# Kernel optimization log

Hardware: AMD Instinct MI355X
Metric: run time of the kernel (lower is better)

The kernel has to match this reference:

```python
import jax, jax.numpy as jnp
import numpy as np

ALPHA = 0.25
GAMMA = 2.0
EPS = 1e-8


def _pairwise_giou_loss(pred, true):
    # pred: (b,1,N,4), true: (b,m,1,4); boxes in [y1,x1,y2,x2] (tfa convention)
    py1, px1, py2, px2 = [pred[..., i] for i in range(4)]
    ty1, tx1, ty2, tx2 = [true[..., i] for i in range(4)]
    p_area = jnp.maximum(py2 - py1, 0.0) * jnp.maximum(px2 - px1, 0.0)
    t_area = jnp.maximum(ty2 - ty1, 0.0) * jnp.maximum(tx2 - tx1, 0.0)
    i_h = jnp.maximum(jnp.minimum(py2, ty2) - jnp.maximum(py1, ty1), 0.0)
    i_w = jnp.maximum(jnp.minimum(px2, tx2) - jnp.maximum(px1, tx1), 0.0)
    inter = i_h * i_w
    union = p_area + t_area - inter
    iou = jnp.where(union > 0, inter / jnp.maximum(union, EPS), 0.0)
    e_h = jnp.maximum(py2, ty2) - jnp.minimum(py1, ty1)
    e_w = jnp.maximum(px2, tx2) - jnp.minimum(px1, tx1)
    enclose = e_h * e_w
    giou = iou - jnp.where(enclose > 0, (enclose - union) / jnp.maximum(enclose, EPS), 0.0)
    return 1.0 - giou  # (b,m,N)


def setup_inputs():
    key = jax.random.key(0)
    k1, k2, k3, k4 = jax.random.split(key, 4)
    b, w, h, c, m = 8, 128, 128, 80, 100
    # probabilities in (0,1) as produced by a sigmoid head
    cls_pred = jax.random.uniform(k1, (b, w, h, c), jnp.float32, 1e-4, 1.0 - 1e-4)
    # raw box coords in grid units (divided by [w,h,w,h] inside the module)
    loc_pred = jax.random.uniform(k2, (b, w, h, 4), jnp.float32) * jnp.asarray([w, h, w, h], jnp.float32)
    labels = jax.random.randint(k3, (b, m), 0, c)
    cls_true = jax.nn.one_hot(labels, c, dtype=jnp.float32)
    loc_true = jax.random.uniform(k4, (b, m, 4), jnp.float32)
    reg_mask = jnp.ones((b, m), jnp.float32)
    return {"cls_pred": cls_pred, "loc_pred": loc_pred, "cls_true": cls_true,
            "loc_true": loc_true, "reg_mask": reg_mask}


def reference(cls_pred, loc_pred, cls_true, loc_true, reg_mask):
    b, w, h, c = cls_pred.shape
    m = cls_true.shape[1]
    cls_true = (cls_true == 1).astype(jnp.float32)
    p = cls_pred.reshape(b, w * h, c)                                      # (b,N,c)
    loc_p = loc_pred.reshape(b, w * h, 4) / jnp.asarray([w, h, w, h], jnp.float32)
    # focal-style pos/neg class costs; contract over c instead of materializing (b,m,N,c)
    neg = (1.0 - ALPHA) * p ** GAMMA * (-jnp.log(1.0 - p + EPS))
    pos = ALPHA * (1.0 - p) ** GAMMA * (-jnp.log(p + EPS))
    cls_loss = jnp.einsum('bnc,bmc->bmn', pos - neg, cls_true)             # (b,m,N)
    reg_loss = jnp.sum(jnp.abs(loc_true[:, :, None, :] - loc_p[:, None, :, :]), axis=-1)
    giou_loss = _pairwise_giou_loss(loc_p[:, None, :, :], loc_true[:, :, None, :])
    total = 2.0 * cls_loss + 5.0 * reg_loss + 2.0 * giou_loss              # (b,m,N)
    argmin_total = jnp.argmin(total, axis=-1).astype(jnp.int32)            # (b,m)
    batch_idx = jnp.broadcast_to(jnp.arange(b, dtype=jnp.int32)[:, None], (b, m))
    cls_id = jnp.argmax(cls_true, axis=-1).astype(jnp.int32)
    return jnp.stack([batch_idx, argmin_total, cls_id], axis=-1)           # (b,m,3) int32
```

## Files before the change

### kernel.cpp

```cpp
#include <hip/hip_runtime.h>
#include <stdint.h>

#define B    8
#define C    80
#define M    100
#define NPIX 16384
#define NT   32
#define BT   128
#define NW   4

#define ALPHA_F 0.25f
#define EPS_F   1e-8f

#define SWZ(c) ((((c) & 31)) ^ ((((c) >> 5)) << 3))

__device__ __forceinline__ uint32_t fkey(float f) {
    uint32_t u = __float_as_uint(f);
    return (u & 0x80000000u) ? ~u : (u | 0x80000000u);
}

__global__ __launch_bounds__(256) void init_kernel(
    const float* __restrict__ cls_true,
    int* __restrict__ cids,
    unsigned long long* __restrict__ keys)
{
    const int bm   = blockIdx.x * NW + (threadIdx.x >> 6);
    const int lane = threadIdx.x & 63;
    if (bm >= B * M) return;

    const float* ct = cls_true + (size_t)bm * C;
    const float v0 = ct[lane];
    unsigned long long k =
        ((unsigned long long)fkey(v0) << 32) | (unsigned int)(C - 1 - lane);
    if (lane + 64 < C) {
        const float v1 = ct[lane + 64];
        unsigned long long k1 =
            ((unsigned long long)fkey(v1) << 32) | (unsigned int)(C - 1 - (lane + 64));
        if (k1 > k) k = k1;
    }
    #pragma unroll
    for (int off = 32; off > 0; off >>= 1) {
        unsigned long long o = __shfl_xor(k, off, 64);
        if (o > k) k = o;
    }
    if (lane == 0) {
        cids[bm] = C - 1 - (int)(k & 0xFFFFFFFFull);
        keys[bm] = 0xFFFFFFFFFFFFFFFFull;
    }
}

__global__ __launch_bounds__(BT, 6) void match_kernel(
    const float* __restrict__ cls_pred,
    const float* __restrict__ loc_pred,
    const float* __restrict__ loc_true,
    const int*   __restrict__ cids,
    unsigned long long* __restrict__ keys)
{
#pragma clang fp contract(off)
    __shared__ float  D[C * NT];
    __shared__ float4 bx4[NT];
    __shared__ float  bpa[NT];

    const int b    = blockIdx.y;
    const int n0   = blockIdx.x * NT;
    const int tid  = threadIdx.x;
    const int lane = tid & 63;
    const int w    = tid >> 6;

    const float4* src4 = (const float4*)(cls_pred + ((size_t)b * NPIX + n0) * C);
    #pragma unroll
    for (int it = 0; it < NT * C / 4 / BT; ++it) {
        const int idx4 = it * BT + tid;
        const int n    = idx4 / 20;
        const int c0   = (idx4 - n * 20) * 4;
        const float4 v = src4[idx4];
        const float pv[4] = { v.x, v.y, v.z, v.w };
        #pragma unroll
        for (int jj = 0; jj < 4; ++jj) {
            const int c = c0 + jj;
            const float p = pv[jj];
            const float q = 1.0f - p;
            const float pos = (ALPHA_F * (q * q)) * (-logf(p + EPS_F));
            const float neg = ((1.0f - ALPHA_F) * (p * p)) * (-logf(q + EPS_F));
            D[c * NT + ((n ^ SWZ(c)) & (NT - 1))] = pos - neg;
        }
    }

    if (tid < NT) {
        const float inv = 1.0f / 128.0f;
        const float4 lp = *(const float4*)(loc_pred + ((size_t)b * NPIX + n0 + tid) * 4);
        const float py1 = lp.x * inv;
        const float px1 = lp.y * inv;
        const float py2 = lp.z * inv;
        const float px2 = lp.w * inv;
        bx4[tid] = make_float4(py1, px1, py2, px2);
        bpa[tid] = fmaxf(py2 - py1, 0.0f) * fmaxf(px2 - px1, 0.0f);
    }

    __syncthreads();

    const int mm = w * 64 + lane;
    if (mm < M) {
        const int bm  = b * M + mm;
        const int cid = cids[bm];
        const float4 lt = *(const float4*)(loc_true + (size_t)bm * 4);
        const float ty1 = lt.x, tx1 = lt.y, ty2 = lt.z, tx2 = lt.w;
        const float t_area = fmaxf(ty2 - ty1, 0.0f) * fmaxf(tx2 - tx1, 0.0f);

        const int drow = cid * NT;
        const int sw   = SWZ(cid) & (NT - 1);

        float bestv = __builtin_huge_valf();
        int   bestn = 0;

        #pragma unroll 8
        for (int j = 0; j < NT; ++j) {
            const float  d  = D[drow + (j ^ sw)];
            const float4 bx = bx4[j];
            const float  pa = bpa[j];
            const float py1 = bx.x, px1 = bx.y, py2 = bx.z, px2 = bx.w;

            const float r = ((fabsf(ty1 - py1) + fabsf(tx1 - px1))
                             + fabsf(ty2 - py2)) + fabsf(tx2 - px2);

            const float ih = fmaxf(fminf(py2, ty2) - fmaxf(py1, ty1), 0.0f);
            const float iw = fmaxf(fminf(px2, tx2) - fmaxf(px1, tx1), 0.0f);
            const float inter = ih * iw;
            const float uni   = (pa + t_area) - inter;
            const float iou   = (uni > 0.0f) ? (inter / fmaxf(uni, EPS_F)) : 0.0f;
            const float eh = fmaxf(py2, ty2) - fminf(py1, ty1);
            const float ew = fmaxf(px2, tx2) - fminf(px1, tx1);
            const float enc = eh * ew;
            const float pen = (enc > 0.0f) ? ((enc - uni) / fmaxf(enc, EPS_F)) : 0.0f;
            const float gl  = 1.0f - (iou - pen);

            const float total = ((2.0f * d) + (5.0f * r)) + (2.0f * gl);

            if (total < bestv) { bestv = total; bestn = n0 + j; }
        }

        const unsigned long long key =
            ((unsigned long long)fkey(bestv) << 32) | (unsigned int)bestn;
        atomicMin(&keys[bm], key);
    }
}

__global__ void write_out_kernel(const unsigned long long* __restrict__ keys,
                                 const int* __restrict__ cids,
                                 int* __restrict__ out) {
    int i = blockIdx.x * blockDim.x + threadIdx.x;
    if (i >= B * M) return;
    out[i * 3 + 0] = i / M;
    out[i * 3 + 1] = (int)(keys[i] & 0xFFFFFFFFull);
    out[i * 3 + 2] = cids[i];
}

extern "C" void kernel_launch(void* const* d_in, const int* in_sizes, int n_in,
                              void* d_out, int out_size, void* d_ws, size_t ws_size,
                              hipStream_t stream) {
    const float* cls_pred = (const float*)d_in[0];
    const float* loc_pred = (const float*)d_in[1];
    const float* cls_true = (const float*)d_in[2];
    const float* loc_true = (const float*)d_in[3];
    int* out = (int*)d_out;

    unsigned long long* keys = (unsigned long long*)d_ws;
    int* cids = (int*)((char*)d_ws + (size_t)B * M * sizeof(unsigned long long));

    init_kernel<<<(B * M + NW - 1) / NW, 256, 0, stream>>>(cls_true, cids, keys);
    match_kernel<<<dim3(NPIX / NT, B), BT, 0, stream>>>(
        cls_pred, loc_pred, loc_true, cids, keys);
    write_out_kernel<<<(B * M + 255) / 256, 256, 0, stream>>>(keys, cids, out);
}
```

Before: 65.78 us.

## Double-buffer class-cost tiles and precompute scaled pred boxes in prep kernel

Each block now handles two 32-pixel tiles. It loads the next tile's class probabilities into registers while it scores the current tile from a double-buffered shared array, so global load latency overlaps with the GIoU compute. Box scaling and area are moved into a separate prep kernel that writes padded 8-float records. The match loop reads those records directly from global memory instead of from shared memory. This adds a kernel launch and a workspace buffer, halves the grid size and drops the occupancy hint from the launch bounds.

```diff
diff --git a/kernel.cpp b/kernel.cpp
--- a/kernel.cpp
+++ b/kernel.cpp
@@ -6,6 +6,7 @@
 #define M    100
 #define NPIX 16384
 #define NT   32
+#define KT   2
 #define BT   128
 #define NW   4
 
@@ -49,96 +50,146 @@
     }
 }
 
-__global__ __launch_bounds__(BT, 6) void match_kernel(
+__global__ __launch_bounds__(256) void prep_kernel(
+    const float* __restrict__ loc_pred,
+    float* __restrict__ pbox)
+{
+#pragma clang fp contract(off)
+    const int i = blockIdx.x * 256 + threadIdx.x;
+    if (i >= B * NPIX) return;
+    const float inv = 1.0f / 128.0f;
+    const float4 lp = ((const float4*)loc_pred)[i];
+    const float py1 = lp.x * inv;
+    const float px1 = lp.y * inv;
+    const float py2 = lp.z * inv;
+    const float px2 = lp.w * inv;
+    const float pa  = fmaxf(py2 - py1, 0.0f) * fmaxf(px2 - px1, 0.0f);
+    float4* dst = (float4*)pbox + (size_t)i * 2;
+    dst[0] = make_float4(py1, px1, py2, px2);
+    dst[1] = make_float4(pa, 0.0f, 0.0f, 0.0f);
+}
+
+__global__ __launch_bounds__(BT) void match_kernel(
     const float* __restrict__ cls_pred,
-    const float* __restrict__ loc_pred,
+    const float* __restrict__ pbox,
     const float* __restrict__ loc_true,
     const int*   __restrict__ cids,
     unsigned long long* __restrict__ keys)
 {
 #pragma clang fp contract(off)
-    __shared__ float  D[C * NT];
-    __shared__ float4 bx4[NT];
-    __shared__ float  bpa[NT];
-
-    const int b    = blockIdx.y;
-    const int n0   = blockIdx.x * NT;
-    const int tid  = threadIdx.x;
-    const int lane = tid & 63;
-    const int w    = tid >> 6;
-
-    const float4* src4 = (const float4*)(cls_pred + ((size_t)b * NPIX + n0) * C);
+    __shared__ float D[2][C * NT];
+
+    const int b      = blockIdx.y;
+    const int base_n = blockIdx.x * (NT * KT);
+    const int tid    = threadIdx.x;
+    const int lane   = tid & 63;
+    const int w      = tid >> 6;
+
+    const int  mm  = w * 64 + lane;
+    const bool act = (mm < M);
+    const int  bm  = b * M + (act ? mm : 0);
+    int cid = 0, drow = 0, sw = 0;
+    float ty1 = 0.f, tx1 = 0.f, ty2 = 0.f, tx2 = 0.f, t_area = 0.f;
+    if (act) {
+        cid = cids[bm];
+        const float4 lt = *(const float4*)(loc_true + (size_t)bm * 4);
+        ty1 = lt.x; tx1 = lt.y; ty2 = lt.z; tx2 = lt.w;
+        t_area = fmaxf(ty2 - ty1, 0.0f) * fmaxf(tx2 - tx1, 0.0f);
+        drow = cid * NT;
+        sw   = SWZ(cid) & (NT - 1);
+    }
+
+    {
+        const float4* src4 = (const float4*)(cls_pred + ((size_t)b * NPIX + base_n) * C);
+        #pragma unroll
+        for (int it = 0; it < NT * C / 4 / BT; ++it) {
+            const int idx4 = it * BT + tid;
+            const int n    = idx4 / 20;
+            const int c0   = (idx4 - n * 20) * 4;
+            const float4 v = src4[idx4];
+            const float pv[4] = { v.x, v.y, v.z, v.w };
+            #pragma unroll
+            for (int jj = 0; jj < 4; ++jj) {
+                const int c = c0 + jj;
+                const float p = pv[jj];
+                const float q = 1.0f - p;
+                const float pos = (ALPHA_F * (q * q)) * (-logf(p + EPS_F));
+                const float neg = ((1.0f - ALPHA_F) * (p * p)) * (-logf(q + EPS_F));
+                D[0][c * NT + ((n ^ SWZ(c)) & (NT - 1))] = pos - neg;
+            }
+        }
+    }
+    __syncthreads();
+
+    float bestv = __builtin_huge_valf();
+    int   bestn = 0;
+
     #pragma unroll
-    for (int it = 0; it < NT * C / 4 / BT; ++it) {
-        const int idx4 = it * BT + tid;
-        const int n    = idx4 / 20;
-        const int c0   = (idx4 - n * 20) * 4;
-        const float4 v = src4[idx4];
-        const float pv[4] = { v.x, v.y, v.z, v.w };
-        #pragma unroll
-        for (int jj = 0; jj < 4; ++jj) {
-            const int c = c0 + jj;
-            const float p = pv[jj];
-            const float q = 1.0f - p;
-            const float pos = (ALPHA_F * (q * q)) * (-logf(p + EPS_F));
-            const float neg = ((1.0f - ALPHA_F) * (p * p)) * (-logf(q + EPS_F));
-            D[c * NT + ((n ^ SWZ(c)) & (NT - 1))] = pos - neg;
-        }
-    }
-
-    if (tid < NT) {
-        const float inv = 1.0f / 128.0f;
-        const float4 lp = *(const float4*)(loc_pred + ((size_t)b * NPIX + n0 + tid) * 4);
-        const float py1 = lp.x * inv;
-        const float px1 = lp.y * inv;
-        const float py2 = lp.z * inv;
-        const float px2 = lp.w * inv;
-        bx4[tid] = make_float4(py1, px1, py2, px2);
-        bpa[tid] = fmaxf(py2 - py1, 0.0f) * fmaxf(px2 - px1, 0.0f);
-    }
-
-    __syncthreads();
-
-    const int mm = w * 64 + lane;
-    if (mm < M) {
-        const int bm  = b * M + mm;
-        const int cid = cids[bm];
-        const float4 lt = *(const float4*)(loc_true + (size_t)bm * 4);
-        const float ty1 = lt.x, tx1 = lt.y, ty2 = lt.z, tx2 = lt.w;
-        const float t_area = fmaxf(ty2 - ty1, 0.0f) * fmaxf(tx2 - tx1, 0.0f);
-
-        const int drow = cid * NT;
-        const int sw   = SWZ(cid) & (NT - 1);
-
-        float bestv = __builtin_huge_valf();
-        int   bestn = 0;
-
-        #pragma unroll 8
-        for (int j = 0; j < NT; ++j) {
-            const float  d  = D[drow + (j ^ sw)];
-            const float4 bx = bx4[j];
-            const float  pa = bpa[j];
-            const float py1 = bx.x, px1 = bx.y, py2 = bx.z, px2 = bx.w;
-
-            const float r = ((fabsf(ty1 - py1) + fabsf(tx1 - px1))
-                             + fabsf(ty2 - py2)) + fabsf(tx2 - px2);
-
-            const float ih = fmaxf(fminf(py2, ty2) - fmaxf(py1, ty1), 0.0f);
-            const float iw = fmaxf(fminf(px2, tx2) - fmaxf(px1, tx1), 0.0f);
-            const float inter = ih * iw;
-            const float uni   = (pa + t_area) - inter;
-            const float iou   = (uni > 0.0f) ? (inter / fmaxf(uni, EPS_F)) : 0.0f;
-            const float eh = fmaxf(py2, ty2) - fminf(py1, ty1);
-            const float ew = fmaxf(px2, tx2) - fminf(px1, tx1);
-            const float enc = eh * ew;
-            const float pen = (enc > 0.0f) ? ((enc - uni) / fmaxf(enc, EPS_F)) : 0.0f;
-            const float gl  = 1.0f - (iou - pen);
-
-            const float total = ((2.0f * d) + (5.0f * r)) + (2.0f * gl);
-
-            if (total < bestv) { bestv = total; bestn = n0 + j; }
-        }
-
+    for (int t = 0; t < KT; ++t) {
+        const int cur = t & 1;
+        const int tn0 = base_n + t * NT;
+
+        float4 ld[5];
+        if (t + 1 < KT) {
+            const float4* src4 =
+                (const float4*)(cls_pred + ((size_t)b * NPIX + tn0 + NT) * C);
+            #pragma unroll
+            for (int it = 0; it < 5; ++it) ld[it] = src4[it * BT + tid];
+        }
+
+        if (act) {
+            const float* pb = pbox + ((size_t)(b * NPIX) + tn0) * 8;
+            #pragma unroll 8
+            for (int j = 0; j < NT; ++j) {
+                const float d   = D[cur][drow + (j ^ sw)];
+                const float py1 = pb[j * 8 + 0];
+                const float px1 = pb[j * 8 + 1];
+                const float py2 = pb[j * 8 + 2];
+                const float px2 = pb[j * 8 + 3];
+                const float pa  = pb[j * 8 + 4];
+
+                const float r = ((fabsf(ty1 - py1) + fabsf(tx1 - px1))
+                                 + fabsf(ty2 - py2)) + fabsf(tx2 - px2);
+
+                const float ih = fmaxf(fminf(py2, ty2) - fmaxf(py1, ty1), 0.0f);
+                const float iw = fmaxf(fminf(px2, tx2) - fmaxf(px1, tx1), 0.0f);
+                const float inter = ih * iw;
+                const float uni   = (pa + t_area) - inter;
+                const float iou   = (uni > 0.0f) ? (inter / fmaxf(uni, EPS_F)) : 0.0f;
+                const float eh = fmaxf(py2, ty2) - fminf(py1, ty1);
+                const float ew = fmaxf(px2, tx2) - fminf(px1, tx1);
+                const float enc = eh * ew;
+                const float pen = (enc > 0.0f) ? ((enc - uni) / fmaxf(enc, EPS_F)) : 0.0f;
+                const float gl  = 1.0f - (iou - pen);
+
+                const float total = ((2.0f * d) + (5.0f * r)) + (2.0f * gl);
+
+                if (total < bestv) { bestv = total; bestn = tn0 + j; }
+            }
+        }
+
+        if (t + 1 < KT) {
+            #pragma unroll
+            for (int it = 0; it < 5; ++it) {
+                const int idx4 = it * BT + tid;
+                const int n    = idx4 / 20;
+                const int c0   = (idx4 - n * 20) * 4;
+                const float pv[4] = { ld[it].x, ld[it].y, ld[it].z, ld[it].w };
+                #pragma unroll
+                for (int jj = 0; jj < 4; ++jj) {
+                    const int c = c0 + jj;
+                    const float p = pv[jj];
+                    const float q = 1.0f - p;
+                    const float pos = (ALPHA_F * (q * q)) * (-logf(p + EPS_F));
+                    const float neg = ((1.0f - ALPHA_F) * (p * p)) * (-logf(q + EPS_F));
+                    D[1 - cur][c * NT + ((n ^ SWZ(c)) & (NT - 1))] = pos - neg;
+                }
+            }
+            __syncthreads();
+        }
+    }
+
+    if (act) {
         const unsigned long long key =
             ((unsigned long long)fkey(bestv) << 32) | (unsigned int)bestn;
         atomicMin(&keys[bm], key);
@@ -165,10 +216,12 @@
     int* out = (int*)d_out;
 
     unsigned long long* keys = (unsigned long long*)d_ws;
-    int* cids = (int*)((char*)d_ws + (size_t)B * M * sizeof(unsigned long long));
+    int*   cids = (int*)((char*)d_ws + (size_t)B * M * sizeof(unsigned long long));
+    float* pbox = (float*)((char*)d_ws + 16384);
 
     init_kernel<<<(B * M + NW - 1) / NW, 256, 0, stream>>>(cls_true, cids, keys);
-    match_kernel<<<dim3(NPIX / NT, B), BT, 0, stream>>>(
-        cls_pred, loc_pred, loc_true, cids, keys);
+    prep_kernel<<<(B * NPIX + 255) / 256, 256, 0, stream>>>(loc_pred, pbox);
+    match_kernel<<<dim3(NPIX / (NT * KT), B), BT, 0, stream>>>(
+        cls_pred, pbox, loc_true, cids, keys);
     write_out_kernel<<<(B * M + 255) / 256, 256, 0, stream>>>(keys, cids, out);
 }
```

Result: faster. 60.33 us (-8.3%).

## Halve pixel tile, use row-major D, and load predicted boxes directly per thread

Applied to the files above, without the earlier changes.

The match kernel tile drops from 32 to 16 pixels per block, which doubles the grid. The swizzled column-major shared class-cost table is replaced by a plain [NT][C] row-major layout filled with float2 stores. The shared staging of predicted boxes and areas is removed, so each thread loads the loc_pred float4s itself (uniform across the wave) and recomputes the pixel area. The ground-truth setup is hoisted above the barrier and the inner loop is fully unrolled. In exchange there are twice as many atomicMin operations, redundant box loads across waves, and possible LDS bank conflicts on the per-thread gather D[j][cid].

```diff
diff --git a/kernel.cpp b/kernel.cpp
--- a/kernel.cpp
+++ b/kernel.cpp
@@ -5,14 +5,12 @@
 #define C    80
 #define M    100
 #define NPIX 16384
-#define NT   32
+#define NT   16
 #define BT   128
 #define NW   4
 
 #define ALPHA_F 0.25f
 #define EPS_F   1e-8f
-
-#define SWZ(c) ((((c) & 31)) ^ ((((c) >> 5)) << 3))
 
 __device__ __forceinline__ uint32_t fkey(float f) {
     uint32_t u = __float_as_uint(f);
@@ -49,7 +47,7 @@
     }
 }
 
-__global__ __launch_bounds__(BT, 6) void match_kernel(
+__global__ __launch_bounds__(BT) void match_kernel(
     const float* __restrict__ cls_pred,
     const float* __restrict__ loc_pred,
     const float* __restrict__ loc_true,
@@ -57,9 +55,7 @@
     unsigned long long* __restrict__ keys)
 {
 #pragma clang fp contract(off)
-    __shared__ float  D[C * NT];
-    __shared__ float4 bx4[NT];
-    __shared__ float  bpa[NT];
+    __shared__ float D[NT][C];
 
     const int b    = blockIdx.y;
     const int n0   = blockIdx.x * NT;
@@ -67,78 +63,72 @@
     const int lane = tid & 63;
     const int w    = tid >> 6;
 
-    const float4* src4 = (const float4*)(cls_pred + ((size_t)b * NPIX + n0) * C);
+    const float2* src2 = (const float2*)(cls_pred + ((size_t)b * NPIX + n0) * C);
     #pragma unroll
-    for (int it = 0; it < NT * C / 4 / BT; ++it) {
-        const int idx4 = it * BT + tid;
-        const int n    = idx4 / 20;
-        const int c0   = (idx4 - n * 20) * 4;
-        const float4 v = src4[idx4];
-        const float pv[4] = { v.x, v.y, v.z, v.w };
+    for (int it = 0; it < NT * C / 2 / BT; ++it) {
+        const int idx2 = it * BT + tid;
+        const int n    = idx2 / 40;
+        const int c0   = (idx2 - n * 40) * 2;
+        const float2 v = src2[idx2];
+        const float pv[2] = { v.x, v.y };
+        float fo[2];
         #pragma unroll
-        for (int jj = 0; jj < 4; ++jj) {
-            const int c = c0 + jj;
+        for (int jj = 0; jj < 2; ++jj) {
             const float p = pv[jj];
             const float q = 1.0f - p;
             const float pos = (ALPHA_F * (q * q)) * (-logf(p + EPS_F));
             const float neg = ((1.0f - ALPHA_F) * (p * p)) * (-logf(q + EPS_F));
-            D[c * NT + ((n ^ SWZ(c)) & (NT - 1))] = pos - neg;
+            fo[jj] = pos - neg;
         }
+        *(float2*)&D[n][c0] = make_float2(fo[0], fo[1]);
     }
 
-    if (tid < NT) {
-        const float inv = 1.0f / 128.0f;
-        const float4 lp = *(const float4*)(loc_pred + ((size_t)b * NPIX + n0 + tid) * 4);
+    const int  mm  = w * 64 + lane;
+    const int  bm  = b * M + (mm < M ? mm : 0);
+    const int  cid = cids[bm];
+    const float4 lt = *(const float4*)(loc_true + (size_t)bm * 4);
+    const float ty1 = lt.x, tx1 = lt.y, ty2 = lt.z, tx2 = lt.w;
+    const float t_area = fmaxf(ty2 - ty1, 0.0f) * fmaxf(tx2 - tx1, 0.0f);
+
+    __syncthreads();
+
+    const float4* lp4 = (const float4*)loc_pred + ((size_t)b * NPIX + n0);
+    const float inv = 1.0f / 128.0f;
+
+    float bestv = __builtin_huge_valf();
+    int   bestn = 0;
+
+    #pragma unroll
+    for (int j = 0; j < NT; ++j) {
+        const float4 lp = lp4[j];
         const float py1 = lp.x * inv;
         const float px1 = lp.y * inv;
         const float py2 = lp.z * inv;
         const float px2 = lp.w * inv;
-        bx4[tid] = make_float4(py1, px1, py2, px2);
-        bpa[tid] = fmaxf(py2 - py1, 0.0f) * fmaxf(px2 - px1, 0.0f);
+        const float pa  = fmaxf(py2 - py1, 0.0f) * fmaxf(px2 - px1, 0.0f);
+
+        const float d = D[j][cid];
+
+        const float r = ((fabsf(ty1 - py1) + fabsf(tx1 - px1))
+                         + fabsf(ty2 - py2)) + fabsf(tx2 - px2);
+
+        const float ih = fmaxf(fminf(py2, ty2) - fmaxf(py1, ty1), 0.0f);
+        const float iw = fmaxf(fminf(px2, tx2) - fmaxf(px1, tx1), 0.0f);
+        const float inter = ih * iw;
+        const float uni   = (pa + t_area) - inter;
+        const float iou   = (uni > 0.0f) ? (inter / fmaxf(uni, EPS_F)) : 0.0f;
+        const float eh = fmaxf(py2, ty2) - fminf(py1, ty1);
+        const float ew = fmaxf(px2, tx2) - fminf(px1, tx1);
+        const float enc = eh * ew;
+        const float pen = (enc > 0.0f) ? ((enc - uni) / fmaxf(enc, EPS_F)) : 0.0f;
+        const float gl  = 1.0f - (iou - pen);
+
+        const float total = ((2.0f * d) + (5.0f * r)) + (2.0f * gl);
+
+        if (total < bestv) { bestv = total; bestn = n0 + j; }
     }
 
-    __syncthreads();
-
-    const int mm = w * 64 + lane;
     if (mm < M) {
-        const int bm  = b * M + mm;
-        const int cid = cids[bm];
-        const float4 lt = *(const float4*)(loc_true + (size_t)bm * 4);
-        const float ty1 = lt.x, tx1 = lt.y, ty2 = lt.z, tx2 = lt.w;
-        const float t_area = fmaxf(ty2 - ty1, 0.0f) * fmaxf(tx2 - tx1, 0.0f);
-
-        const int drow = cid * NT;
-        const int sw   = SWZ(cid) & (NT - 1);
-
-        float bestv = __builtin_huge_valf();
-        int   bestn = 0;
-
-        #pragma unroll 8
-        for (int j = 0; j < NT; ++j) {
-            const float  d  = D[drow + (j ^ sw)];
-            const float4 bx = bx4[j];
-            const float  pa = bpa[j];
-            const float py1 = bx.x, px1 = bx.y, py2 = bx.z, px2 = bx.w;
-
-            const float r = ((fabsf(ty1 - py1) + fabsf(tx1 - px1))
-                             + fabsf(ty2 - py2)) + fabsf(tx2 - px2);
-
-            const float ih = fmaxf(fminf(py2, ty2) - fmaxf(py1, ty1), 0.0f);
-            const float iw = fmaxf(fminf(px2, tx2) - fmaxf(px1, tx1), 0.0f);
-            const float inter = ih * iw;
-            const float uni   = (pa + t_area) - inter;
-            const float iou   = (uni > 0.0f) ? (inter / fmaxf(uni, EPS_F)) : 0.0f;
-            const float eh = fmaxf(py2, ty2) - fminf(py1, ty1);
-            const float ew = fmaxf(px2, tx2) - fminf(px1, tx1);
-            const float enc = eh * ew;
-            const float pen = (enc > 0.0f) ? ((enc - uni) / fmaxf(enc, EPS_F)) : 0.0f;
-            const float gl  = 1.0f - (iou - pen);
-
-            const float total = ((2.0f * d) + (5.0f * r)) + (2.0f * gl);
-
-            if (total < bestv) { bestv = total; bestn = n0 + j; }
-        }
-
         const unsigned long long key =
             ((unsigned long long)fkey(bestv) << 32) | (unsigned int)bestn;
         atomicMin(&keys[bm], key);
```

Measured after the change: 106.8 us. +62.3%, slower.

## Enlarge pixel tile, split match work across waves, precompute pred boxes in prep kernel

Applied to the files above, without the earlier changes.

The pixel tile grows from 32 to 128 per block and the block from 128 to 256 threads. Two wave pairs each scan half the tile for the same 100 targets, so each block issues fewer atomicMin operations and the block count drops by four. Predicted boxes and their areas are now normalized once by a new prep kernel into a workspace buffer. The match loop reads them from global memory (wave-uniform, so scalar or cached loads) instead of shared memory. This adds a kernel launch and extra global traffic. The last 28 lanes of the second wave now do wasted work, and occupancy may drop because of the larger shared tile.

```diff
diff --git a/kernel.cpp b/kernel.cpp
--- a/kernel.cpp
+++ b/kernel.cpp
@@ -5,8 +5,8 @@
 #define C    80
 #define M    100
 #define NPIX 16384
-#define NT   32
-#define BT   128
+#define NT   128
+#define BT   256
 #define NW   4
 
 #define ALPHA_F 0.25f
@@ -49,17 +49,34 @@
     }
 }
 
-__global__ __launch_bounds__(BT, 6) void match_kernel(
+__global__ __launch_bounds__(256) void prep_kernel(
+    const float* __restrict__ loc_pred,
+    float* __restrict__ pbox)
+{
+#pragma clang fp contract(off)
+    const int i = blockIdx.x * 256 + threadIdx.x;
+    if (i >= B * NPIX) return;
+    const float inv = 1.0f / 128.0f;
+    const float4 lp = ((const float4*)loc_pred)[i];
+    const float py1 = lp.x * inv;
+    const float px1 = lp.y * inv;
+    const float py2 = lp.z * inv;
+    const float px2 = lp.w * inv;
+    const float pa  = fmaxf(py2 - py1, 0.0f) * fmaxf(px2 - px1, 0.0f);
+    float4* dst = (float4*)pbox + (size_t)i * 2;
+    dst[0] = make_float4(py1, px1, py2, px2);
+    dst[1] = make_float4(pa, 0.0f, 0.0f, 0.0f);
+}
+
+__global__ __launch_bounds__(BT) void match_kernel(
     const float* __restrict__ cls_pred,
-    const float* __restrict__ loc_pred,
+    const float* __restrict__ pbox,
     const float* __restrict__ loc_true,
     const int*   __restrict__ cids,
     unsigned long long* __restrict__ keys)
 {
 #pragma clang fp contract(off)
-    __shared__ float  D[C * NT];
-    __shared__ float4 bx4[NT];
-    __shared__ float  bpa[NT];
+    __shared__ float D[C * NT];
 
     const int b    = blockIdx.y;
     const int n0   = blockIdx.x * NT;
@@ -86,59 +103,53 @@
         }
     }
 
-    if (tid < NT) {
-        const float inv = 1.0f / 128.0f;
-        const float4 lp = *(const float4*)(loc_pred + ((size_t)b * NPIX + n0 + tid) * 4);
-        const float py1 = lp.x * inv;
-        const float px1 = lp.y * inv;
-        const float py2 = lp.z * inv;
-        const float px2 = lp.w * inv;
-        bx4[tid] = make_float4(py1, px1, py2, px2);
-        bpa[tid] = fmaxf(py2 - py1, 0.0f) * fmaxf(px2 - px1, 0.0f);
-    }
+    const int  mm  = (w & 1) * 64 + lane;
+    const int  bm  = b * M + (mm < M ? mm : 0);
+    const int  cid = cids[bm];
+    const float4 lt = *(const float4*)(loc_true + (size_t)bm * 4);
+    const float ty1 = lt.x, tx1 = lt.y, ty2 = lt.z, tx2 = lt.w;
+    const float t_area = fmaxf(ty2 - ty1, 0.0f) * fmaxf(tx2 - tx1, 0.0f);
+    const int drow = cid * NT;
+    const int sw   = SWZ(cid);
 
     __syncthreads();
 
-    const int mm = w * 64 + lane;
+    const int jbase = (w >> 1) * 64;
+    const float* pb = pbox + ((size_t)(b * NPIX) + n0 + jbase) * 8;
+
+    float bestv = __builtin_huge_valf();
+    int   bestn = 0;
+
+    #pragma unroll 8
+    for (int j = 0; j < 64; ++j) {
+        const int cell = jbase + j;
+        const float d   = D[drow + (cell ^ sw)];
+        const float py1 = pb[j * 8 + 0];
+        const float px1 = pb[j * 8 + 1];
+        const float py2 = pb[j * 8 + 2];
+        const float px2 = pb[j * 8 + 3];
+        const float pa  = pb[j * 8 + 4];
+
+        const float r = ((fabsf(ty1 - py1) + fabsf(tx1 - px1))
+                         + fabsf(ty2 - py2)) + fabsf(tx2 - px2);
+
+        const float ih = fmaxf(fminf(py2, ty2) - fmaxf(py1, ty1), 0.0f);
+        const float iw = fmaxf(fminf(px2, tx2) - fmaxf(px1, tx1), 0.0f);
+        const float inter = ih * iw;
+        const float uni   = (pa + t_area) - inter;
+        const float iou   = (uni > 0.0f) ? (inter / fmaxf(uni, EPS_F)) : 0.0f;
+        const float eh = fmaxf(py2, ty2) - fminf(py1, ty1);
+        const float ew = fmaxf(px2, tx2) - fminf(px1, tx1);
+        const float enc = eh * ew;
+        const float pen = (enc > 0.0f) ? ((enc - uni) / fmaxf(enc, EPS_F)) : 0.0f;
+        const float gl  = 1.0f - (iou - pen);
+
+        const float total = ((2.0f * d) + (5.0f * r)) + (2.0f * gl);
+
+        if (total < bestv) { bestv = total; bestn = n0 + cell; }
+    }
+
     if (mm < M) {
-        const int bm  = b * M + mm;
-        const int cid = cids[bm];
-        const float4 lt = *(const float4*)(loc_true + (size_t)bm * 4);
-        const float ty1 = lt.x, tx1 = lt.y, ty2 = lt.z, tx2 = lt.w;
-        const float t_area = fmaxf(ty2 - ty1, 0.0f) * fmaxf(tx2 - tx1, 0.0f);
-
-        const int drow = cid * NT;
-        const int sw   = SWZ(cid) & (NT - 1);
-
-        float bestv = __builtin_huge_valf();
-        int   bestn = 0;
-
-        #pragma unroll 8
-        for (int j = 0; j < NT; ++j) {
-            const float  d  = D[drow + (j ^ sw)];
-            const float4 bx = bx4[j];
-            const float  pa = bpa[j];
-            const float py1 = bx.x, px1 = bx.y, py2 = bx.z, px2 = bx.w;
-
-            const float r = ((fabsf(ty1 - py1) + fabsf(tx1 - px1))
-                             + fabsf(ty2 - py2)) + fabsf(tx2 - px2);
-
-            const float ih = fmaxf(fminf(py2, ty2) - fmaxf(py1, ty1), 0.0f);
-            const float iw = fmaxf(fminf(px2, tx2) - fmaxf(px1, tx1), 0.0f);
-            const float inter = ih * iw;
-            const float uni   = (pa + t_area) - inter;
-            const float iou   = (uni > 0.0f) ? (inter / fmaxf(uni, EPS_F)) : 0.0f;
-            const float eh = fmaxf(py2, ty2) - fminf(py1, ty1);
-            const float ew = fmaxf(px2, tx2) - fminf(px1, tx1);
-            const float enc = eh * ew;
-            const float pen = (enc > 0.0f) ? ((enc - uni) / fmaxf(enc, EPS_F)) : 0.0f;
-            const float gl  = 1.0f - (iou - pen);
-
-            const float total = ((2.0f * d) + (5.0f * r)) + (2.0f * gl);
-
-            if (total < bestv) { bestv = total; bestn = n0 + j; }
-        }
-
         const unsigned long long key =
             ((unsigned long long)fkey(bestv) << 32) | (unsigned int)bestn;
         atomicMin(&keys[bm], key);
@@ -165,10 +176,12 @@
     int* out = (int*)d_out;
 
     unsigned long long* keys = (unsigned long long*)d_ws;
-    int* cids = (int*)((char*)d_ws + (size_t)B * M * sizeof(unsigned long long));
+    int*   cids = (int*)((char*)d_ws + (size_t)B * M * sizeof(unsigned long long));
+    float* pbox = (float*)((char*)d_ws + 16384);
 
     init_kernel<<<(B * M + NW - 1) / NW, 256, 0, stream>>>(cls_true, cids, keys);
+    prep_kernel<<<(B * NPIX + 255) / 256, 256, 0, stream>>>(loc_pred, pbox);
     match_kernel<<<dim3(NPIX / NT, B), BT, 0, stream>>>(
-        cls_pred, loc_pred, loc_true, cids, keys);
+        cls_pred, pbox, loc_true, cids, keys);
     write_out_kernel<<<(B * M + 255) / 256, 256, 0, stream>>>(keys, cids, out);
 }
```

Measured after the change: 65.84 us. No clear change (+0.1%).
